# Performance work log

Measured on AMD Instinct MI355X. Metric: run time of the kernel, lower is better.

Reference implementation:

```python
import jax, jax.numpy as jnp
import numpy as np

NUM_HEADS = 4
KERNEL = 7
DILATION = 1
EMBED = 128
CTX = 256
RANK = 8
HEAD_DIM = EMBED // NUM_HEADS
SCALE = HEAD_DIM ** (-0.5)


def setup_inputs() -> dict:
    key = jax.random.key(0)
    ks = jax.random.split(key, 16)
    B, H, W = 4, 64, 64
    inp = {
        "x": jax.random.normal(ks[0], (B, H, W, EMBED), jnp.float32),
        "context": jax.random.normal(ks[1], (B, CTX), jnp.float32),
        # base QKV linear (torch Linear: y = x @ W.T + b)
        "Wqkv": jax.random.normal(ks[2], (3 * EMBED, EMBED), jnp.float32) * 0.02,
        "bqkv": jax.random.normal(ks[3], (3 * EMBED,), jnp.float32) * 0.02,
        # bilinear LoRA params (init scale 0.01 as in source)
        "A": jax.random.normal(ks[4], (EMBED, RANK), jnp.float32) * 0.01,
        "Blora": jax.random.normal(ks[5], (CTX, RANK), jnp.float32) * 0.01,
        "Vlora": jax.random.normal(ks[6], (3 * EMBED, RANK), jnp.float32) * 0.01,
        # gate MLP: Linear(ctx,16) -> ReLU -> Linear(16,1) -> Sigmoid
        "g1w": jax.random.normal(ks[7], (16, CTX), jnp.float32) * 0.05,
        "g1b": jnp.zeros((16,), jnp.float32),
        "g2w": jnp.full((1, 16), -5.0, jnp.float32) * 0.0 + jax.random.normal(ks[8], (1, 16), jnp.float32) * 0.01 - 5.0 / 16.0,
        "g2b": jnp.full((1,), -5.0, jnp.float32),
        # output projection
        "Wproj": jax.random.normal(ks[9], (EMBED, EMBED), jnp.float32) * 0.02,
        "bproj": jnp.zeros((EMBED,), jnp.float32),
    }
    return inp


def _windows(t, H, W):
    # t: [B, nh, H+2p, W+2p, d] -> [B, nh, H, W, K^2, d]
    ws = []
    for i in range(KERNEL):
        for j in range(KERNEL):
            ws.append(t[:, :, i * DILATION:i * DILATION + H, j * DILATION:j * DILATION + W, :])
    return jnp.stack(ws, axis=4)


def reference(x, context, Wqkv, bqkv, A, Blora, Vlora, g1w, g1b, g2w, g2b, Wproj, bproj):
    B, H, W, C = x.shape
    nh, hd = NUM_HEADS, HEAD_DIM
    # context-modulated QKV: base + alpha * ((xA) * (cB)) V^T
    base = x @ Wqkv.T + bqkv                                   # [B,H,W,3C]
    c_proj = context @ Blora                                   # [B,r]
    delta = ((x @ A) * c_proj[:, None, None, :]) @ Vlora.T     # [B,H,W,3C]
    alpha = jax.nn.sigmoid(jax.nn.relu(context @ g1w.T + g1b) @ g2w.T + g2b)  # [B,1]
    qkv = base + alpha[:, None, None, :] * delta               # [B,H,W,3C]

    qkv = qkv.reshape(B, H, W, 3, nh, hd)
    qkv = jnp.transpose(qkv, (3, 0, 4, 1, 2, 5))               # [3,B,nh,H,W,hd]
    q, k, v = qkv[0], qkv[1], qkv[2]

    pad = DILATION * (KERNEL - 1) // 2
    pw = ((0, 0), (0, 0), (pad, pad), (pad, pad), (0, 0))
    k_p = jnp.pad(k, pw)
    v_p = jnp.pad(v, pw)
    kw = _windows(k_p, H, W)                                   # [B,nh,H,W,K2,hd]
    vw = _windows(v_p, H, W)

    attn = jnp.einsum('bnijd,bnijkd->bnijk', q, kw) * SCALE    # [B,nh,H,W,K2]
    attn = jax.nn.softmax(attn, axis=-1)
    out = jnp.einsum('bnijk,bnijkd->bnijd', attn, vw)          # [B,nh,H,W,hd]

    out = jnp.transpose(out, (0, 2, 3, 1, 4)).reshape(B, H, W, C)
    out = out @ Wproj.T + bproj
    return out
```

## Files before the change

kernel.cpp:

```cpp
#include <hip/hip_runtime.h>
#include <cstddef>

#define CTXDIM 256
#define RANK 8
#define SCALE 0.17677669529663687f
#define WSTRIDE 136

#define WF0 0
#define QS0 8704
#define KL0 17408
#define VT0 53248
#define SMSZ 77824
#define KHEAD 8960
#define VHEAD 8192

typedef _Float16 half8 __attribute__((ext_vector_type(8)));
typedef _Float16 half2_t __attribute__((ext_vector_type(2)));
typedef float floatx4 __attribute__((ext_vector_type(4)));
typedef float floatx16 __attribute__((ext_vector_type(16)));
typedef int intx4 __attribute__((ext_vector_type(4)));

struct Params {
  const float *x, *ctx, *Wqkv, *bqkv, *A, *Blora, *Vlora;
  const float *g1w, *g1b, *g2w, *g2b, *Wproj, *bproj;
  float* out;
};

__device__ __forceinline__ void stage_rows_f16_512(const float* __restrict__ src,
                                                   _Float16* dst, int tid) {
  const int row = tid >> 2;
  const int c0 = (tid & 3) * 32;
  const float* sp = src + (size_t)row * 128 + c0;
  _Float16* dp = dst + row * WSTRIDE + c0;
#pragma unroll
  for (int i = 0; i < 4; ++i) {
    const float4 a = *(const float4*)(sp + i * 8);
    const float4 b = *(const float4*)(sp + i * 8 + 4);
    half8 o;
    o[0] = (_Float16)a.x; o[1] = (_Float16)a.y;
    o[2] = (_Float16)a.z; o[3] = (_Float16)a.w;
    o[4] = (_Float16)b.x; o[5] = (_Float16)b.y;
    o[6] = (_Float16)b.z; o[7] = (_Float16)b.w;
    *(half8*)(dp + i * 8) = o;
  }
}

__device__ __forceinline__ int vta(int d, int k) {
  const int sig = (d + (d >> 3)) & 7;
  return d * 256 + (((k >> 3) ^ sig) << 3) + (k & 7);
}

__device__ __forceinline__ int packh(float x, float y) {
  half2_t h;
  h[0] = (_Float16)x;
  h[1] = (_Float16)y;
  return __builtin_bit_cast(int, h);
}

template <int MT0>
__device__ __forceinline__ floatx16 attn_wave(const _Float16* kls,
                                              const _Float16* vtl,
                                              half8 qb0, half8 qb1,
                                              int m31, int l5, int pi, int pj) {
  const floatx16 zz = {0.f,0.f,0.f,0.f,0.f,0.f,0.f,0.f,
                       0.f,0.f,0.f,0.f,0.f,0.f,0.f,0.f};
  floatx16 acc[5];
#pragma unroll
  for (int mt = 0; mt < 5; ++mt) {
    const int Mt = MT0 + mt;
    const half8 ka0 = *(const half8*)&kls[(Mt * 32 + m31) * 40 + l5 * 8];
    const half8 ka1 = *(const half8*)&kls[(Mt * 32 + m31) * 40 + 16 + l5 * 8];
    floatx16 a = zz;
    a = __builtin_amdgcn_mfma_f32_32x32x16_f16(ka0, qb0, a, 0, 0, 0);
    a = __builtin_amdgcn_mfma_f32_32x32x16_f16(ka1, qb1, a, 0, 0, 0);
    acc[mt] = a;
  }

  bool vR[14];
#pragma unroll
  for (int i = 0; i < 14; ++i) vR[i] = (unsigned)(i - pi) < 7u;
  bool vC[8];
#pragma unroll
  for (int c8 = 0; c8 < 8; ++c8) {
    const int hcv = (c8 & 3) + 8 * (c8 >> 2) + 4 * l5;
    vC[c8] = (unsigned)(hcv - pj) < 7u;
  }

  float mxp[4] = {-1e30f, -1e30f, -1e30f, -1e30f};
#pragma unroll
  for (int mt = 0; mt < 5; ++mt) {
#pragma unroll
    for (int reg = 0; reg < 16; ++reg) {
      const bool v = vR[2 * (MT0 + mt) + (reg >> 3)] &&
                     vC[(reg & 3) + 4 * ((reg >> 2) & 1)];
      const float x = v ? acc[mt][reg] : -1e30f;
      acc[mt][reg] = x;
      mxp[reg & 3] = fmaxf(mxp[reg & 3], x);
    }
  }
  float mx = fmaxf(fmaxf(mxp[0], mxp[1]), fmaxf(mxp[2], mxp[3]));
  mx = fmaxf(mx, __shfl_xor(mx, 32, 64));

  const float SC2 = SCALE * 1.4426950408889634f;
  float sp[4] = {0.f, 0.f, 0.f, 0.f};
#pragma unroll
  for (int mt = 0; mt < 5; ++mt) {
#pragma unroll
    for (int reg = 0; reg < 16; ++reg) {
      const float pv = exp2f((acc[mt][reg] - mx) * SC2);
      acc[mt][reg] = pv;
      sp[reg & 3] += pv;
    }
  }
  float sum = (sp[0] + sp[1]) + (sp[2] + sp[3]);
  sum += __shfl_xor(sum, 32, 64);
  const float inv = 1.f / sum;

  floatx16 oacc = zz;
  const int sigd = (m31 + (m31 >> 3)) & 7;
  const int vbase = m31 * 256;
#pragma unroll
  for (int kk = 0; kk < 10; ++kk) {
    const int ks = MT0 * 2 + kk;
    const int mt = (ks >> 1) - MT0;
    const int r8 = 8 * (ks & 1);
    const int E00 = packh(acc[mt][r8 + 0] * inv, acc[mt][r8 + 1] * inv);
    const int E01 = packh(acc[mt][r8 + 2] * inv, acc[mt][r8 + 3] * inv);
    const int E10 = packh(acc[mt][r8 + 4] * inv, acc[mt][r8 + 5] * inv);
    const int E11 = packh(acc[mt][r8 + 6] * inv, acc[mt][r8 + 7] * inv);
    const int R00 = __shfl_xor(E00, 32, 64);
    const int R01 = __shfl_xor(E01, 32, 64);
    const int R10 = __shfl_xor(E10, 32, 64);
    const int R11 = __shfl_xor(E11, 32, 64);
    const int A0 = l5 ? R10 : E00;
    const int A1 = l5 ? R11 : E01;
    const int A2 = l5 ? E10 : R00;
    const int A3 = l5 ? E11 : R01;
    const intx4 ai = {A0, A1, A2, A3};
    const half8 af = __builtin_bit_cast(half8, ai);
    const half8 vb = *(const half8*)&vtl[vbase + (((2 * ks + l5) ^ sigd) << 3)];
    oacc = __builtin_amdgcn_mfma_f32_32x32x16_f16(af, vb, oacc, 0, 0, 0);
  }
  return oacc;
}

__global__ __launch_bounds__(512, 1) void mono_kernel(Params p) {
  __shared__ __align__(16) _Float16 sm[SMSZ];

  const int bid = blockIdx.x;
  const int tj = bid & 7;
  const int ti = (bid >> 3) & 7;
  const int b  = bid >> 6;
  const int tid = threadIdx.x;
  const int lane = tid & 63;
  const int w = tid >> 6;
  const int m31 = lane & 31;
  const int l5 = lane >> 5;
  const int i0 = ti * 8 - 3;
  const int j0 = tj * 8 - 3;

  _Float16* wfold = sm + WF0;
  _Float16* qs    = sm + QS0;
  _Float16* kls   = sm + KL0;
  _Float16* vtl   = sm + VT0;

  const floatx16 zz = {0.f,0.f,0.f,0.f,0.f,0.f,0.f,0.f,
                       0.f,0.f,0.f,0.f,0.f,0.f,0.f,0.f};
  const int sigd = (m31 + (m31 >> 3)) & 7;

  auto load_xrow = [&](int rowlin, half8* xr) {
#pragma unroll
    for (int ks = 0; ks < 8; ++ks) xr[ks] = (half8){0, 0, 0, 0, 0, 0, 0, 0};
    if (rowlin < 196) {
      const int hr = rowlin / 14;
      const int hc = rowlin - hr * 14;
      const int ii = i0 + hr;
      const int jj = j0 + hc;
      if ((unsigned)ii < 64u && (unsigned)jj < 64u) {
        const float* xp = p.x + (size_t)(b * 4096 + ii * 64 + jj) * 128 + l5 * 8;
#pragma unroll
        for (int ks = 0; ks < 8; ++ks) {
          const float4 a = *(const float4*)(xp + ks * 16);
          const float4 c = *(const float4*)(xp + ks * 16 + 4);
          half8 o;
          o[0] = (_Float16)a.x; o[1] = (_Float16)a.y;
          o[2] = (_Float16)a.z; o[3] = (_Float16)a.w;
          o[4] = (_Float16)c.x; o[5] = (_Float16)c.y;
          o[6] = (_Float16)c.z; o[7] = (_Float16)c.w;
          xr[ks] = o;
        }
      }
    }
  };

  const int mtq = (w & 3) + 1;
  const int chq = w >> 2;
  half8 xrq[8];
  load_xrow(mtq * 32 + m31, xrq);

  float calr[RANK];
  {
    const float c0 = p.ctx[b * CTXDIM + lane];
    const float c1 = p.ctx[b * CTXDIM + 64 + lane];
    const float c2 = p.ctx[b * CTXDIM + 128 + lane];
    const float c3 = p.ctx[b * CTXDIM + 192 + lane];
    float cp[RANK];
#pragma unroll
    for (int r = 0; r < RANK; ++r) {
      float q = c0 * p.Blora[lane * RANK + r] + c1 * p.Blora[(64 + lane) * RANK + r] +
                c2 * p.Blora[(128 + lane) * RANK + r] + c3 * p.Blora[(192 + lane) * RANK + r];
#pragma unroll
      for (int s = 32; s; s >>= 1) q += __shfl_xor(q, s, 64);
      cp[r] = q;
    }
    float gacc = 0.f;
#pragma unroll
    for (int h = 0; h < 16; ++h) {
      float q = c0 * p.g1w[h * CTXDIM + lane] + c1 * p.g1w[h * CTXDIM + 64 + lane] +
                c2 * p.g1w[h * CTXDIM + 128 + lane] + c3 * p.g1w[h * CTXDIM + 192 + lane];
#pragma unroll
      for (int s = 32; s; s >>= 1) q += __shfl_xor(q, s, 64);
      gacc += fmaxf(q + p.g1b[h], 0.f) * p.g2w[h];
    }
    const float alpha = 1.f / (1.f + __expf(-(gacc + p.g2b[0])));
#pragma unroll
    for (int r = 0; r < RANK; ++r) calr[r] = alpha * cp[r];
  }

  for (int idx = tid; idx < 2688; idx += 512) {
    const int hd = idx / 896;
    const int r2 = idx - hd * 896;
    const int d = r2 & 31;
    const int kk = r2 >> 5;
    const int k = (kk >> 1) * 16 + 14 + (kk & 1);
    vtl[hd * VHEAD + vta(d, k)] = (_Float16)0.f;
  }

  const int kq = tid & 127;
  const int hgrp = tid >> 7;
  const float4 a0 = *(const float4*)&p.A[kq * RANK];
  const float4 a1 = *(const float4*)&p.A[kq * RANK + 4];

  __syncthreads();

  const float t0 = a0.x * calr[0], t1 = a0.y * calr[1];
  const float t2 = a0.z * calr[2], t3 = a0.w * calr[3];
  const float t4 = a1.x * calr[4], t5 = a1.y * calr[5];
  const float t6 = a1.z * calr[6], t7 = a1.w * calr[7];

  auto FOLD = [&](int n0) {
#pragma unroll
    for (int rr = 0; rr < 16; ++rr) {
      const int row = hgrp * 16 + rr;
      const int o = n0 + row;
      const float4 v0 = *(const float4*)&p.Vlora[o * RANK];
      const float4 v1 = *(const float4*)&p.Vlora[o * RANK + 4];
      float d = t0 * v0.x;
      d = fmaf(t1, v0.y, d);
      d = fmaf(t2, v0.z, d);
      d = fmaf(t3, v0.w, d);
      d = fmaf(t4, v1.x, d);
      d = fmaf(t5, v1.y, d);
      d = fmaf(t6, v1.z, d);
      d = fmaf(t7, v1.w, d);
      wfold[row * WSTRIDE + kq] = (_Float16)(p.Wqkv[o * 128 + kq] + d);
    }
  };

  auto QGEMM = [&](int i) {
    const int n0 = i * 64;
    const int nc = n0 + chq * 32 + m31;
    const float bq = p.bqkv[nc];
    floatx16 c = zz;
    const _Float16* br = &wfold[(chq * 32 + m31) * WSTRIDE + l5 * 8];
#pragma unroll
    for (int ks = 0; ks < 8; ++ks) {
      const half8 f = *(const half8*)(br + ks * 16);
      c = __builtin_amdgcn_mfma_f32_32x32x16_f16(xrq[ks], f, c, 0, 0, 0);
    }
#pragma unroll
    for (int reg = 0; reg < 16; ++reg) {
      const int rowlin = mtq * 32 + (reg & 3) + 8 * (reg >> 2) + 4 * l5;
      const int hr = rowlin / 14;
      const int hc = rowlin - hr * 14;
      if ((unsigned)(hr - 3) < 8u && (unsigned)(hc - 3) < 8u) {
        const int px = (hr - 3) * 8 + (hc - 3);
        qs[px * 136 + nc] = (_Float16)(c[reg] + bq);
      }
    }
  };

  FOLD(0);   __syncthreads(); QGEMM(0); __syncthreads();
  FOLD(64);  __syncthreads(); QGEMM(1); __syncthreads();

  half8 xrkv[8];
  load_xrow(w * 32 + m31, xrkv);
  floatx16 v3save = zz;

  auto KVGEMM = [&](int it) {
    const int n0 = it * 64;
    const float bh0 = p.bqkv[n0 + m31];
    const float bh1 = p.bqkv[n0 + 32 + m31];
    if (w < 7) {
      floatx16 c0 = zz, c1 = zz;
      const _Float16* b0r = &wfold[m31 * WSTRIDE + l5 * 8];
      const _Float16* b1r = &wfold[(32 + m31) * WSTRIDE + l5 * 8];
#pragma unroll
      for (int ks = 0; ks < 8; ++ks) {
        const half8 f0 = *(const half8*)(b0r + ks * 16);
        const half8 f1 = *(const half8*)(b1r + ks * 16);
        c0 = __builtin_amdgcn_mfma_f32_32x32x16_f16(xrkv[ks], f0, c0, 0, 0, 0);
        c1 = __builtin_amdgcn_mfma_f32_32x32x16_f16(xrkv[ks], f1, c1, 0, 0, 0);
      }
#pragma unroll
      for (int reg = 0; reg < 16; ++reg) {
        const int rowlin = w * 32 + (reg & 3) + 8 * (reg >> 2) + 4 * l5;
        if (rowlin < 196) {
          const int hr = rowlin / 14;
          const int hc = rowlin - hr * 14;
          const int hp = hr * 16 + hc;
          const bool ok = (unsigned)(i0 + hr) < 64u && (unsigned)(j0 + hc) < 64u;
          const float v0 = ok ? c0[reg] + bh0 : 0.f;
          const float v1 = ok ? c1[reg] + bh1 : 0.f;
          const int off = (((hp >> 3) ^ sigd) << 3) | (hp & 7);
          if (it == 2) {
            kls[hp * 40 + m31] = (_Float16)v0;
            kls[KHEAD + hp * 40 + m31] = (_Float16)v1;
          } else if (it == 3) {
            kls[2 * KHEAD + hp * 40 + m31] = (_Float16)v0;
            kls[3 * KHEAD + hp * 40 + m31] = (_Float16)v1;
          } else if (it == 4) {
            vtl[m31 * 256 + off] = (_Float16)v0;
            vtl[VHEAD + m31 * 256 + off] = (_Float16)v1;
          } else {
            vtl[2 * VHEAD + m31 * 256 + off] = (_Float16)v0;
            v3save[reg] = v1;
          }
        }
      }
    }
  };

  FOLD(128); __syncthreads(); KVGEMM(2); __syncthreads();
  FOLD(192); __syncthreads(); KVGEMM(3); __syncthreads();
  FOLD(256); __syncthreads(); KVGEMM(4); __syncthreads();
  FOLD(320); __syncthreads(); KVGEMM(5); __syncthreads();

  for (int idx = tid; idx < 896; idx += 512) {
    const int d = idx & 31;
    const int kk = idx >> 5;
    const int k = (kk >> 1) * 16 + 14 + (kk & 1);
    wfold[vta(d, k)] = (_Float16)0.f;
  }
  if (w < 7) {
#pragma unroll
    for (int reg = 0; reg < 16; ++reg) {
      const int rowlin = w * 32 + (reg & 3) + 8 * (reg >> 2) + 4 * l5;
      if (rowlin < 196) {
        const int hr = rowlin / 14;
        const int hc = rowlin - hr * 14;
        const int hp = hr * 16 + hc;
        const int off = (((hp >> 3) ^ sigd) << 3) | (hp & 7);
        wfold[m31 * 256 + off] = (_Float16)v3save[reg];
      }
    }
  }
  __syncthreads();

  const int hh = w >> 1;
  const int half_ = w & 1;
  const int pixA = half_ * 32 + m31;
  const int piA = pixA >> 3, pjA = pixA & 7;
  const half8 qb0 = *(const half8*)&qs[pixA * 136 + hh * 32 + l5 * 8];
  const half8 qb1 = *(const half8*)&qs[pixA * 136 + hh * 32 + 16 + l5 * 8];
  const _Float16* kpp = kls + hh * KHEAD;
  const _Float16* vpp = (hh < 3) ? (vtl + hh * VHEAD) : wfold;

  const floatx16 oA = half_ ? attn_wave<2>(kpp, vpp, qb0, qb1, m31, l5, piA, pjA)
                            : attn_wave<0>(kpp, vpp, qb0, qb1, m31, l5, piA, pjA);
  __syncthreads();

  _Float16* at_s = kls;
  _Float16* wsh  = kls + 64 * WSTRIDE;
#pragma unroll
  for (int reg = 0; reg < 16; ++reg) {
    const int rowM = (reg & 3) + 8 * (reg >> 2) + 4 * l5;
    at_s[(half_ * 32 + rowM) * WSTRIDE + hh * 32 + m31] = (_Float16)oA[reg];
  }
  stage_rows_f16_512(p.Wproj, wsh, tid);
  __syncthreads();

  const int r = lane & 15;
  const int quad = lane >> 4;
  const int rw = w & 3;
  const int nh = w >> 2;
  const _Float16* ap = at_s + (rw * 16 + r) * WSTRIDE + quad * 8;
  const _Float16* bp = wsh + (nh * 64 + r) * WSTRIDE + quad * 8;
  floatx4 acc[4];
#pragma unroll
  for (int nt = 0; nt < 4; ++nt) acc[nt] = (floatx4){0.f, 0.f, 0.f, 0.f};
#pragma unroll
  for (int kc = 0; kc < 4; ++kc) {
    const half8 a = *(const half8*)(ap + kc * 32);
#pragma unroll
    for (int nt = 0; nt < 4; ++nt) {
      const half8 bf = *(const half8*)(bp + nt * 16 * WSTRIDE + kc * 32);
      acc[nt] = __builtin_amdgcn_mfma_f32_16x16x32_f16(a, bf, acc[nt], 0, 0, 0);
    }
  }

  const int rbase = b * 4096 + (ti * 8 + rw * 2 + (quad >> 1)) * 64 +
                    tj * 8 + (quad & 1) * 4;
  float bv[4];
#pragma unroll
  for (int nt = 0; nt < 4; ++nt) bv[nt] = p.bproj[nh * 64 + nt * 16 + r];
#pragma unroll
  for (int reg = 0; reg < 4; ++reg) {
    float* cp = p.out + (size_t)(rbase + reg) * 128 + nh * 64;
#pragma unroll
    for (int nt = 0; nt < 4; ++nt)
      cp[nt * 16 + r] = acc[nt][reg] + bv[nt];
  }
}

extern "C" void kernel_launch(void* const* d_in, const int* in_sizes, int n_in,
                              void* d_out, int out_size, void* d_ws, size_t ws_size,
                              hipStream_t stream) {
  Params hp;
  hp.x     = (const float*)d_in[0];
  hp.ctx   = (const float*)d_in[1];
  hp.Wqkv  = (const float*)d_in[2];
  hp.bqkv  = (const float*)d_in[3];
  hp.A     = (const float*)d_in[4];
  hp.Blora = (const float*)d_in[5];
  hp.Vlora = (const float*)d_in[6];
  hp.g1w   = (const float*)d_in[7];
  hp.g1b   = (const float*)d_in[8];
  hp.g2w   = (const float*)d_in[9];
  hp.g2b   = (const float*)d_in[10];
  hp.Wproj = (const float*)d_in[11];
  hp.bproj = (const float*)d_in[12];
  hp.out   = (float*)d_out;

  mono_kernel<<<256, 512, 0, stream>>>(hp);
}
```

Measured before the change: 48.46 us.

## Split heads across two blocks per tile and reduce projection with atomics

Each spatial tile is now handled by two 256-thread blocks, each computing two of the four heads (QKV fold, attention, partial output projection). The partial projection results are accumulated into the output with atomicAdd after a memset, and shared memory per block is roughly halved so two blocks can fit per CU. This is meant to increase parallelism and occupancy, at the cost of doing the x loads and ctx/gate math twice, an extra memset launch, and atomic traffic on the output.

Result: slower. 59.65 us (+23.1%).

```diff
diff --git a/kernel.cpp b/kernel.cpp
--- a/kernel.cpp
+++ b/kernel.cpp
@@ -4,15 +4,18 @@
 #define CTXDIM 256
 #define RANK 8
 #define SCALE 0.17677669529663687f
-#define WSTRIDE 136
-
-#define WF0 0
-#define QS0 8704
-#define KL0 17408
-#define VT0 53248
-#define SMSZ 77824
+
+#define WFSTR 136
+#define QSTR  68
+#define ATSTR 72
+#define KSTR  40
 #define KHEAD 8960
 #define VHEAD 8192
+
+#define WF0 0
+#define KL0 4352
+#define VT0 22272
+#define SMSZ 38656
 
 typedef _Float16 half8 __attribute__((ext_vector_type(8)));
 typedef _Float16 half2_t __attribute__((ext_vector_type(2)));
@@ -25,25 +28,6 @@
   const float *g1w, *g1b, *g2w, *g2b, *Wproj, *bproj;
   float* out;
 };
-
-__device__ __forceinline__ void stage_rows_f16_512(const float* __restrict__ src,
-                                                   _Float16* dst, int tid) {
-  const int row = tid >> 2;
-  const int c0 = (tid & 3) * 32;
-  const float* sp = src + (size_t)row * 128 + c0;
-  _Float16* dp = dst + row * WSTRIDE + c0;
-#pragma unroll
-  for (int i = 0; i < 4; ++i) {
-    const float4 a = *(const float4*)(sp + i * 8);
-    const float4 b = *(const float4*)(sp + i * 8 + 4);
-    half8 o;
-    o[0] = (_Float16)a.x; o[1] = (_Float16)a.y;
-    o[2] = (_Float16)a.z; o[3] = (_Float16)a.w;
-    o[4] = (_Float16)b.x; o[5] = (_Float16)b.y;
-    o[6] = (_Float16)b.z; o[7] = (_Float16)b.w;
-    *(half8*)(dp + i * 8) = o;
-  }
-}
 
 __device__ __forceinline__ int vta(int d, int k) {
   const int sig = (d + (d >> 3)) & 7;
@@ -68,8 +52,8 @@
 #pragma unroll
   for (int mt = 0; mt < 5; ++mt) {
     const int Mt = MT0 + mt;
-    const half8 ka0 = *(const half8*)&kls[(Mt * 32 + m31) * 40 + l5 * 8];
-    const half8 ka1 = *(const half8*)&kls[(Mt * 32 + m31) * 40 + 16 + l5 * 8];
+    const half8 ka0 = *(const half8*)&kls[(Mt * 32 + m31) * KSTR + l5 * 8];
+    const half8 ka1 = *(const half8*)&kls[(Mt * 32 + m31) * KSTR + 16 + l5 * 8];
     floatx16 a = zz;
     a = __builtin_amdgcn_mfma_f32_32x32x16_f16(ka0, qb0, a, 0, 0, 0);
     a = __builtin_amdgcn_mfma_f32_32x32x16_f16(ka1, qb1, a, 0, 0, 0);
@@ -144,13 +128,15 @@
   return oacc;
 }
 
-__global__ __launch_bounds__(512, 1) void mono_kernel(Params p) {
+__global__ __launch_bounds__(256, 2) void mono_kernel(Params p) {
   __shared__ __align__(16) _Float16 sm[SMSZ];
 
   const int bid = blockIdx.x;
-  const int tj = bid & 7;
-  const int ti = (bid >> 3) & 7;
-  const int b  = bid >> 6;
+  const int hp = bid >> 8;
+  const int tile = bid & 255;
+  const int tj = tile & 7;
+  const int ti = (tile >> 3) & 7;
+  const int b  = tile >> 6;
   const int tid = threadIdx.x;
   const int lane = tid & 63;
   const int w = tid >> 6;
@@ -160,7 +146,7 @@
   const int j0 = tj * 8 - 3;
 
   _Float16* wfold = sm + WF0;
-  _Float16* qs    = sm + QS0;
+  _Float16* qs    = sm + WF0;
   _Float16* kls   = sm + KL0;
   _Float16* vtl   = sm + VT0;
 
@@ -193,9 +179,10 @@
     }
   };
 
-  const int mtq = (w & 3) + 1;
-  const int chq = w >> 2;
-  half8 xrq[8];
+  const int mtq = (w == 0) ? 4 : w;
+  half8 xrA[8], xrB[8], xrq[8];
+  load_xrow(w * 32 + m31, xrA);
+  load_xrow((w + 4) * 32 + m31, xrB);
   load_xrow(mtq * 32 + m31, xrq);
 
   float calr[RANK];
@@ -227,7 +214,7 @@
     for (int r = 0; r < RANK; ++r) calr[r] = alpha * cp[r];
   }
 
-  for (int idx = tid; idx < 2688; idx += 512) {
+  for (int idx = tid; idx < 1792; idx += 256) {
     const int hd = idx / 896;
     const int r2 = idx - hd * 896;
     const int d = r2 & 31;
@@ -240,19 +227,16 @@
   const int hgrp = tid >> 7;
   const float4 a0 = *(const float4*)&p.A[kq * RANK];
   const float4 a1 = *(const float4*)&p.A[kq * RANK + 4];
-
-  __syncthreads();
-
   const float t0 = a0.x * calr[0], t1 = a0.y * calr[1];
   const float t2 = a0.z * calr[2], t3 = a0.w * calr[3];
   const float t4 = a1.x * calr[4], t5 = a1.y * calr[5];
   const float t6 = a1.z * calr[6], t7 = a1.w * calr[7];
 
-  auto FOLD = [&](int n0) {
+  auto FOLD = [&](int nb) {
 #pragma unroll
     for (int rr = 0; rr < 16; ++rr) {
       const int row = hgrp * 16 + rr;
-      const int o = n0 + row;
+      const int o = nb + row;
       const float4 v0 = *(const float4*)&p.Vlora[o * RANK];
       const float4 v1 = *(const float4*)&p.Vlora[o * RANK + 4];
       float d = t0 * v0.x;
@@ -263,169 +247,175 @@
       d = fmaf(t5, v1.y, d);
       d = fmaf(t6, v1.z, d);
       d = fmaf(t7, v1.w, d);
-      wfold[row * WSTRIDE + kq] = (_Float16)(p.Wqkv[o * 128 + kq] + d);
+      wfold[row * WFSTR + kq] = (_Float16)(p.Wqkv[o * 128 + kq] + d);
     }
   };
 
-  auto QGEMM = [&](int i) {
-    const int n0 = i * 64;
-    const int nc = n0 + chq * 32 + m31;
-    const float bq = p.bqkv[nc];
-    floatx16 c = zz;
-    const _Float16* br = &wfold[(chq * 32 + m31) * WSTRIDE + l5 * 8];
+  auto KVG2 = [&](int nb, int sub, bool isK) {
+    floatx16 cA = zz, cB = zz;
+    const _Float16* br = &wfold[m31 * WFSTR + l5 * 8];
 #pragma unroll
     for (int ks = 0; ks < 8; ++ks) {
       const half8 f = *(const half8*)(br + ks * 16);
-      c = __builtin_amdgcn_mfma_f32_32x32x16_f16(xrq[ks], f, c, 0, 0, 0);
-    }
-#pragma unroll
-    for (int reg = 0; reg < 16; ++reg) {
-      const int rowlin = mtq * 32 + (reg & 3) + 8 * (reg >> 2) + 4 * l5;
-      const int hr = rowlin / 14;
-      const int hc = rowlin - hr * 14;
-      if ((unsigned)(hr - 3) < 8u && (unsigned)(hc - 3) < 8u) {
-        const int px = (hr - 3) * 8 + (hc - 3);
-        qs[px * 136 + nc] = (_Float16)(c[reg] + bq);
-      }
-    }
-  };
-
-  FOLD(0);   __syncthreads(); QGEMM(0); __syncthreads();
-  FOLD(64);  __syncthreads(); QGEMM(1); __syncthreads();
-
-  half8 xrkv[8];
-  load_xrow(w * 32 + m31, xrkv);
-  floatx16 v3save = zz;
-
-  auto KVGEMM = [&](int it) {
-    const int n0 = it * 64;
-    const float bh0 = p.bqkv[n0 + m31];
-    const float bh1 = p.bqkv[n0 + 32 + m31];
-    if (w < 7) {
-      floatx16 c0 = zz, c1 = zz;
-      const _Float16* b0r = &wfold[m31 * WSTRIDE + l5 * 8];
-      const _Float16* b1r = &wfold[(32 + m31) * WSTRIDE + l5 * 8];
-#pragma unroll
-      for (int ks = 0; ks < 8; ++ks) {
-        const half8 f0 = *(const half8*)(b0r + ks * 16);
-        const half8 f1 = *(const half8*)(b1r + ks * 16);
-        c0 = __builtin_amdgcn_mfma_f32_32x32x16_f16(xrkv[ks], f0, c0, 0, 0, 0);
-        c1 = __builtin_amdgcn_mfma_f32_32x32x16_f16(xrkv[ks], f1, c1, 0, 0, 0);
-      }
-#pragma unroll
-      for (int reg = 0; reg < 16; ++reg) {
-        const int rowlin = w * 32 + (reg & 3) + 8 * (reg >> 2) + 4 * l5;
-        if (rowlin < 196) {
-          const int hr = rowlin / 14;
-          const int hc = rowlin - hr * 14;
-          const int hp = hr * 16 + hc;
-          const bool ok = (unsigned)(i0 + hr) < 64u && (unsigned)(j0 + hc) < 64u;
-          const float v0 = ok ? c0[reg] + bh0 : 0.f;
-          const float v1 = ok ? c1[reg] + bh1 : 0.f;
-          const int off = (((hp >> 3) ^ sigd) << 3) | (hp & 7);
-          if (it == 2) {
-            kls[hp * 40 + m31] = (_Float16)v0;
-            kls[KHEAD + hp * 40 + m31] = (_Float16)v1;
-          } else if (it == 3) {
-            kls[2 * KHEAD + hp * 40 + m31] = (_Float16)v0;
-            kls[3 * KHEAD + hp * 40 + m31] = (_Float16)v1;
-          } else if (it == 4) {
-            vtl[m31 * 256 + off] = (_Float16)v0;
-            vtl[VHEAD + m31 * 256 + off] = (_Float16)v1;
-          } else {
-            vtl[2 * VHEAD + m31 * 256 + off] = (_Float16)v0;
-            v3save[reg] = v1;
+      cA = __builtin_amdgcn_mfma_f32_32x32x16_f16(xrA[ks], f, cA, 0, 0, 0);
+      cB = __builtin_amdgcn_mfma_f32_32x32x16_f16(xrB[ks], f, cB, 0, 0, 0);
+    }
+    const float bh = p.bqkv[nb + m31];
+#pragma unroll
+    for (int half2x = 0; half2x < 2; ++half2x) {
+      const int mt = w + 4 * half2x;
+      if (mt < 7) {
+        const floatx16 cc = half2x ? cB : cA;
+#pragma unroll
+        for (int reg = 0; reg < 16; ++reg) {
+          const int rl = mt * 32 + (reg & 3) + 8 * (reg >> 2) + 4 * l5;
+          if (rl < 196) {
+            const int hr = rl / 14;
+            const int hc = rl - hr * 14;
+            const int hpx = hr * 16 + hc;
+            const bool ok = (unsigned)(i0 + hr) < 64u && (unsigned)(j0 + hc) < 64u;
+            const float v = ok ? cc[reg] + bh : 0.f;
+            if (isK) {
+              kls[sub * KHEAD + hpx * KSTR + m31] = (_Float16)v;
+            } else {
+              const int off = (((hpx >> 3) ^ sigd) << 3) | (hpx & 7);
+              vtl[sub * VHEAD + m31 * 256 + off] = (_Float16)v;
+            }
           }
         }
       }
     }
   };
 
-  FOLD(128); __syncthreads(); KVGEMM(2); __syncthreads();
-  FOLD(192); __syncthreads(); KVGEMM(3); __syncthreads();
-  FOLD(256); __syncthreads(); KVGEMM(4); __syncthreads();
-  FOLD(320); __syncthreads(); KVGEMM(5); __syncthreads();
-
-  for (int idx = tid; idx < 896; idx += 512) {
-    const int d = idx & 31;
-    const int kk = idx >> 5;
-    const int k = (kk >> 1) * 16 + 14 + (kk & 1);
-    wfold[vta(d, k)] = (_Float16)0.f;
-  }
-  if (w < 7) {
+  auto QG = [&](floatx16& cq) {
+    cq = zz;
+    const _Float16* br = &wfold[m31 * WFSTR + l5 * 8];
+#pragma unroll
+    for (int ks = 0; ks < 8; ++ks) {
+      const half8 f = *(const half8*)(br + ks * 16);
+      cq = __builtin_amdgcn_mfma_f32_32x32x16_f16(xrq[ks], f, cq, 0, 0, 0);
+    }
+  };
+
+  const int nK = (2 + hp) * 64;
+  const int nV = (4 + hp) * 64;
+  const int nQ = hp * 64;
+
+  FOLD(nK);                 __syncthreads();
+  KVG2(nK, 0, true);        __syncthreads();
+  FOLD(nK + 32);            __syncthreads();
+  KVG2(nK + 32, 1, true);   __syncthreads();
+  FOLD(nV);                 __syncthreads();
+  KVG2(nV, 0, false);       __syncthreads();
+  FOLD(nV + 32);            __syncthreads();
+  KVG2(nV + 32, 1, false);  __syncthreads();
+  floatx16 cQ0, cQ1;
+  FOLD(nQ);                 __syncthreads();
+  QG(cQ0);                  __syncthreads();
+  FOLD(nQ + 32);            __syncthreads();
+  QG(cQ1);                  __syncthreads();
+
+  {
+    const float bq0 = p.bqkv[nQ + m31];
+    const float bq1 = p.bqkv[nQ + 32 + m31];
 #pragma unroll
     for (int reg = 0; reg < 16; ++reg) {
-      const int rowlin = w * 32 + (reg & 3) + 8 * (reg >> 2) + 4 * l5;
-      if (rowlin < 196) {
-        const int hr = rowlin / 14;
-        const int hc = rowlin - hr * 14;
-        const int hp = hr * 16 + hc;
-        const int off = (((hp >> 3) ^ sigd) << 3) | (hp & 7);
-        wfold[m31 * 256 + off] = (_Float16)v3save[reg];
+      const int rl = mtq * 32 + (reg & 3) + 8 * (reg >> 2) + 4 * l5;
+      const int hr = rl / 14;
+      const int hc = rl - hr * 14;
+      if ((unsigned)(hr - 3) < 8u && (unsigned)(hc - 3) < 8u) {
+        const int px = (hr - 3) * 8 + (hc - 3);
+        qs[px * QSTR + m31]      = (_Float16)(cQ0[reg] + bq0);
+        qs[px * QSTR + 32 + m31] = (_Float16)(cQ1[reg] + bq1);
       }
     }
   }
   __syncthreads();
 
-  const int hh = w >> 1;
+  const int hl = w >> 1;
   const int half_ = w & 1;
   const int pixA = half_ * 32 + m31;
   const int piA = pixA >> 3, pjA = pixA & 7;
-  const half8 qb0 = *(const half8*)&qs[pixA * 136 + hh * 32 + l5 * 8];
-  const half8 qb1 = *(const half8*)&qs[pixA * 136 + hh * 32 + 16 + l5 * 8];
-  const _Float16* kpp = kls + hh * KHEAD;
-  const _Float16* vpp = (hh < 3) ? (vtl + hh * VHEAD) : wfold;
+  half8 qb0, qb1;
+  {
+    const _Float16* qp = qs + pixA * QSTR + hl * 32 + l5 * 8;
+#pragma unroll
+    for (int e = 0; e < 4; ++e) {
+      const half2_t v0 = *(const half2_t*)(qp + 2 * e);
+      const half2_t v1 = *(const half2_t*)(qp + 16 + 2 * e);
+      qb0[2 * e] = v0[0]; qb0[2 * e + 1] = v0[1];
+      qb1[2 * e] = v1[0]; qb1[2 * e + 1] = v1[1];
+    }
+  }
+  const _Float16* kpp = kls + hl * KHEAD;
+  const _Float16* vpp = vtl + hl * VHEAD;
 
   const floatx16 oA = half_ ? attn_wave<2>(kpp, vpp, qb0, qb1, m31, l5, piA, pjA)
                             : attn_wave<0>(kpp, vpp, qb0, qb1, m31, l5, piA, pjA);
   __syncthreads();
 
-  _Float16* at_s = kls;
-  _Float16* wsh  = kls + 64 * WSTRIDE;
+  _Float16* at_s = sm + KL0;
+  _Float16* wsh  = sm + KL0 + 64 * ATSTR;
 #pragma unroll
   for (int reg = 0; reg < 16; ++reg) {
     const int rowM = (reg & 3) + 8 * (reg >> 2) + 4 * l5;
-    at_s[(half_ * 32 + rowM) * WSTRIDE + hh * 32 + m31] = (_Float16)oA[reg];
-  }
-  stage_rows_f16_512(p.Wproj, wsh, tid);
+    at_s[(half_ * 32 + rowM) * ATSTR + hl * 32 + m31] = (_Float16)oA[reg];
+  }
+  {
+    const int row = tid >> 1;
+    const int cs = (tid & 1) * 32;
+    const float* spp = p.Wproj + (size_t)row * 128 + hp * 64 + cs;
+    _Float16* dpp = wsh + row * ATSTR + cs;
+#pragma unroll
+    for (int i2 = 0; i2 < 4; ++i2) {
+      const float4 a = *(const float4*)(spp + i2 * 8);
+      const float4 c = *(const float4*)(spp + i2 * 8 + 4);
+      half8 o;
+      o[0] = (_Float16)a.x; o[1] = (_Float16)a.y;
+      o[2] = (_Float16)a.z; o[3] = (_Float16)a.w;
+      o[4] = (_Float16)c.x; o[5] = (_Float16)c.y;
+      o[6] = (_Float16)c.z; o[7] = (_Float16)c.w;
+      *(half8*)(dpp + i2 * 8) = o;
+    }
+  }
   __syncthreads();
 
   const int r = lane & 15;
   const int quad = lane >> 4;
-  const int rw = w & 3;
-  const int nh = w >> 2;
-  const _Float16* ap = at_s + (rw * 16 + r) * WSTRIDE + quad * 8;
-  const _Float16* bp = wsh + (nh * 64 + r) * WSTRIDE + quad * 8;
-  floatx4 acc[4];
-#pragma unroll
-  for (int nt = 0; nt < 4; ++nt) acc[nt] = (floatx4){0.f, 0.f, 0.f, 0.f};
-#pragma unroll
-  for (int kc = 0; kc < 4; ++kc) {
+  const _Float16* ap = at_s + (w * 16 + r) * ATSTR + quad * 8;
+  const _Float16* bp = wsh + r * ATSTR + quad * 8;
+  floatx4 acc[8];
+#pragma unroll
+  for (int nt = 0; nt < 8; ++nt) acc[nt] = (floatx4){0.f, 0.f, 0.f, 0.f};
+#pragma unroll
+  for (int kc = 0; kc < 2; ++kc) {
     const half8 a = *(const half8*)(ap + kc * 32);
 #pragma unroll
-    for (int nt = 0; nt < 4; ++nt) {
-      const half8 bf = *(const half8*)(bp + nt * 16 * WSTRIDE + kc * 32);
+    for (int nt = 0; nt < 8; ++nt) {
+      const half8 bf = *(const half8*)(bp + nt * 16 * ATSTR + kc * 32);
       acc[nt] = __builtin_amdgcn_mfma_f32_16x16x32_f16(a, bf, acc[nt], 0, 0, 0);
     }
   }
 
-  const int rbase = b * 4096 + (ti * 8 + rw * 2 + (quad >> 1)) * 64 +
+  const int rbase = b * 4096 + (ti * 8 + w * 2 + (quad >> 1)) * 64 +
                     tj * 8 + (quad & 1) * 4;
-  float bv[4];
-#pragma unroll
-  for (int nt = 0; nt < 4; ++nt) bv[nt] = p.bproj[nh * 64 + nt * 16 + r];
+  float bv[8];
+#pragma unroll
+  for (int nt = 0; nt < 8; ++nt) bv[nt] = hp ? 0.f : p.bproj[nt * 16 + r];
 #pragma unroll
   for (int reg = 0; reg < 4; ++reg) {
-    float* cp = p.out + (size_t)(rbase + reg) * 128 + nh * 64;
-#pragma unroll
-    for (int nt = 0; nt < 4; ++nt)
-      cp[nt * 16 + r] = acc[nt][reg] + bv[nt];
+    float* cp = p.out + (size_t)(rbase + reg) * 128;
+#pragma unroll
+    for (int nt = 0; nt < 8; ++nt)
+      atomicAdd(&cp[nt * 16 + r], acc[nt][reg] + bv[nt]);
   }
 }
 
 extern "C" void kernel_launch(void* const* d_in, const int* in_sizes, int n_in,
                               void* d_out, int out_size, void* d_ws, size_t ws_size,
                               hipStream_t stream) {
+  hipMemsetAsync(d_out, 0, (size_t)out_size * sizeof(float), stream);
+
   Params hp;
   hp.x     = (const float*)d_in[0];
   hp.ctx   = (const float*)d_in[1];
@@ -442,5 +432,5 @@
   hp.bproj = (const float*)d_in[12];
   hp.out   = (float*)d_out;
 
-  mono_kernel<<<256, 512, 0, stream>>>(hp);
+  mono_kernel<<<512, 256, 0, stream>>>(hp);
 }
```
